# Optimization experiments

Measured on AMD Instinct MI355X. Metric: run time of the kernel, lower is better.

The kernel has to match this reference:

```python
import jax, jax.numpy as jnp
import numpy as np

MIN_V, MAX_V = 1e-7, 10.0
POWER = 2.0
N_NODES = 200000


def _hyper_layer(H, edges, W, b):
    """One HyperTensorGraphConvolution layer (full-neighborhood branch).

    H: [N, d] node signals; edges: [E, S] node indices per hyperedge.
    For each (edge, node_i): power-mean over the other S-1 nodes of the edge,
    divided by (S-1), accumulated onto node_i; then row-normalize and linear.
    """
    N, d = H.shape
    E, S = edges.shape
    H = jnp.clip(H, MIN_V, MAX_V)
    P = H ** POWER                                   # [N, d]
    g = P[edges]                                     # [E, S, d] gather
    edge_sum = g.sum(axis=1, keepdims=True)          # [E, 1, d]
    neigh_mean = (edge_sum - g) / (S - 1)            # exclude self, /(len(nodes)-1)
    contrib = neigh_mean ** (1.0 / POWER)            # [E, S, d]
    add = jax.ops.segment_sum(contrib.reshape(E * S, d),
                              edges.reshape(-1), num_segments=N)
    new_signal = H + add
    # row-normalize (rowsum > 0 because H >= 1e-7)
    rowsum = new_signal.sum(axis=1)
    r_inv = jnp.where(jnp.isfinite(1.0 / rowsum), 1.0 / rowsum, 0.0)
    AH = new_signal * r_inv[:, None]
    return AH @ W + b


def setup_inputs() -> dict:
    key = jax.random.key(0)
    k1, k2, k3, k4, k5, k6 = jax.random.split(key, 6)
    d, h, c = 128, 16, 40
    H = jax.random.uniform(k1, (N_NODES, d), dtype=jnp.float32)
    edges = jax.random.randint(k2, (40000, 16), 0, N_NODES, dtype=jnp.int64)
    std1 = 1.0 / np.sqrt(h)
    std2 = 1.0 / np.sqrt(c)
    W1 = jax.random.uniform(k3, (d, h), jnp.float32, -std1, std1)
    b1 = jax.random.uniform(k4, (h,), jnp.float32, -std1, std1)
    W2 = jax.random.uniform(k5, (h, c), jnp.float32, -std2, std2)
    b2 = jax.random.uniform(k6, (c,), jnp.float32, -std2, std2)
    return {"H": H, "W1": W1, "b1": b1, "W2": W2, "b2": b2, "edges": edges}


def reference(H, W1, b1, W2, b2, edges):
    # layer 1 + relu (dropout is identity in eval mode)
    x = jax.nn.relu(_hyper_layer(H, edges, W1, b1))
    # layer 2
    return _hyper_layer(x, edges, W2, b2)
```

## Files before the change

### kernel.cpp

```cpp
#include <hip/hip_runtime.h>

#define MIN_V 1e-7f
#define MAX_V 10.0f
#define INV15 (1.0f/15.0f)
#define CAP 32

typedef _Float16 half2v __attribute__((ext_vector_type(2)));
typedef _Float16 half4v __attribute__((ext_vector_type(4)));
typedef _Float16 half8v __attribute__((ext_vector_type(8)));

static __device__ __forceinline__ float clipv(float v){
    return fminf(fmaxf(v, MIN_V), MAX_V);
}
static __device__ __forceinline__ float rsqrt_arg(float v){
    return __builtin_amdgcn_sqrtf(fmaxf(v, 0.f));
}

__global__ __launch_bounds__(256) void ch_stream(const float* __restrict__ H,
                                                 _Float16* __restrict__ CH, int total8){
    int stride = gridDim.x*256;
    for (int i = blockIdx.x*256 + threadIdx.x; i < total8; i += stride){
        const float4* p = (const float4*)(H + (size_t)i*8);
        float4 a = p[0], b = p[1];
        half8v o;
        o[0]=(_Float16)clipv(a.x); o[1]=(_Float16)clipv(a.y);
        o[2]=(_Float16)clipv(a.z); o[3]=(_Float16)clipv(a.w);
        o[4]=(_Float16)clipv(b.x); o[5]=(_Float16)clipv(b.y);
        o[6]=(_Float16)clipv(b.z); o[7]=(_Float16)clipv(b.w);
        *(half8v*)(CH + (size_t)i*8) = o;
    }
}

__global__ void build_lists(const int* __restrict__ edges, int* __restrict__ cnt,
                            unsigned short* __restrict__ lists, int total){
    int i = blockIdx.x*256 + threadIdx.x;
    if (i >= total) return;
    int node = edges[i];
    int p = atomicAdd(&cnt[node], 1);
    if (p < CAP) lists[(size_t)node*CAP + p] = (unsigned short)(i >> 4);
}

__global__ __launch_bounds__(256) void es_l1(const _Float16* __restrict__ CH,
                                             const int* __restrict__ edges,
                                             _Float16* __restrict__ ES1s, int E){
    int wave = threadIdx.x >> 6, lane = threadIdx.x & 63;
    int e = blockIdx.x*4 + wave;
    if (e >= E) return;
    int rid = edges[(size_t)e*16 + (lane & 15)];
    float s0 = 0.f, s1 = 0.f;
    #pragma unroll
    for (int s=0;s<16;++s){
        int idx = __shfl(rid, s, 64);
        half2v v = *(const half2v*)(CH + (size_t)idx*128 + lane*2);
        float f0 = (float)v[0], f1 = (float)v[1];
        s0 += f0*f0; s1 += f1*f1;
    }
    half2v o; o[0] = (_Float16)(s0*INV15); o[1] = (_Float16)(s1*INV15);
    *(half2v*)(ES1s + (size_t)e*128 + lane*2) = o;
}

__global__ __launch_bounds__(256) void fused_l1(
    const _Float16* __restrict__ CH, const _Float16* __restrict__ ES1s,
    const int* __restrict__ cnt, const unsigned short* __restrict__ lists,
    const float* __restrict__ W1, const float* __restrict__ b1,
    _Float16* __restrict__ X, int N){
    __shared__ float snw[8*144];
    int tid = threadIdx.x;
    int wave = tid >> 6, lane = tid & 63;

    int q = lane >> 4, h = lane & 15;
    float w[32];
    #pragma unroll
    for (int i=0;i<32;++i) w[i] = W1[(q*32+i)*16 + h];
    float bv = b1[h];

    int hw = tid >> 5;
    int k32 = tid & 31;
    int dq = k32 * 4;

    int nb = blockIdx.x * 8;

    int n = nb + hw;
    if (n < N){
        int myid = (int)lists[(size_t)n*CAP + k32];
        int len = cnt[n]; if (len > CAP) len = CAP;

        half4v hv = *(const half4v*)(CH + (size_t)n*128 + dq);
        float h0=(float)hv[0], h1=(float)hv[1], h2=(float)hv[2], h3=(float)hv[3];
        float p0=h0*h0*INV15, p1=h1*h1*INV15, p2=h2*h2*INV15, p3=h3*h3*INV15;

        float a0=0.f, a1=0.f, a2=0.f, a3=0.f;
        for (int k0=0;k0<len;k0+=4){
            int e0 = __shfl(myid, k0+0, 32);
            int e1 = __shfl(myid, k0+1, 32);
            int e2 = __shfl(myid, k0+2, 32);
            int e3 = __shfl(myid, k0+3, 32);
            half4v v0 = *(const half4v*)(ES1s + (size_t)e0*128 + dq);
            half4v v1 = *(const half4v*)(ES1s + (size_t)e1*128 + dq);
            half4v v2 = *(const half4v*)(ES1s + (size_t)e2*128 + dq);
            half4v v3 = *(const half4v*)(ES1s + (size_t)e3*128 + dq);
            a0 += rsqrt_arg((float)v0[0] - p0);
            a1 += rsqrt_arg((float)v0[1] - p1);
            a2 += rsqrt_arg((float)v0[2] - p2);
            a3 += rsqrt_arg((float)v0[3] - p3);
            bool m1 = (k0+1 < len), m2 = (k0+2 < len), m3 = (k0+3 < len);
            a0 += m1 ? rsqrt_arg((float)v1[0] - p0) : 0.f;
            a1 += m1 ? rsqrt_arg((float)v1[1] - p1) : 0.f;
            a2 += m1 ? rsqrt_arg((float)v1[2] - p2) : 0.f;
            a3 += m1 ? rsqrt_arg((float)v1[3] - p3) : 0.f;
            a0 += m2 ? rsqrt_arg((float)v2[0] - p0) : 0.f;
            a1 += m2 ? rsqrt_arg((float)v2[1] - p1) : 0.f;
            a2 += m2 ? rsqrt_arg((float)v2[2] - p2) : 0.f;
            a3 += m2 ? rsqrt_arg((float)v2[3] - p3) : 0.f;
            a0 += m3 ? rsqrt_arg((float)v3[0] - p0) : 0.f;
            a1 += m3 ? rsqrt_arg((float)v3[1] - p1) : 0.f;
            a2 += m3 ? rsqrt_arg((float)v3[2] - p2) : 0.f;
            a3 += m3 ? rsqrt_arg((float)v3[3] - p3) : 0.f;
        }
        float4 wv;
        wv.x = h0+a0; wv.y = h1+a1; wv.z = h2+a2; wv.w = h3+a3;
        *(float4*)&snw[hw*144 + (k32>>3)*36 + (k32&7)*4] = wv;
    }
    __syncthreads();

    #pragma unroll
    for (int r=0;r<2;++r){
        int nl = wave*2 + r;
        int n2 = nb + nl;
        if (n2 >= N) continue;
        float acc = 0.f, rs = 0.f;
        #pragma unroll
        for (int j=0;j<8;++j){
            float4 v = *(const float4*)&snw[nl*144 + q*36 + j*4];
            acc += v.x*w[j*4+0] + v.y*w[j*4+1] + v.z*w[j*4+2] + v.w*w[j*4+3];
            rs  += v.x + v.y + v.z + v.w;
        }
        acc += __shfl_xor(acc, 16, 64);
        rs  += __shfl_xor(rs , 16, 64);
        acc += __shfl_xor(acc, 32, 64);
        rs  += __shfl_xor(rs , 32, 64);
        if (q == 0){
            float o = acc * __builtin_amdgcn_rcpf(rs) + bv;
            X[(size_t)n2*16 + h] = (_Float16)fmaxf(o, 0.f);
        }
    }
}

__global__ __launch_bounds__(256) void es_l2(const _Float16* __restrict__ X,
                                             const int* __restrict__ edges,
                                             _Float16* __restrict__ ES2s, int E){
    int t = blockIdx.x*256 + threadIdx.x;
    int e = t >> 3, dd2 = (t & 7)*2;
    if (e >= E) return;
    const int* row = edges + (size_t)e*16;
    float s0 = 0.f, s1 = 0.f;
    #pragma unroll
    for (int s=0;s<16;++s){
        half2v v = *(const half2v*)(X + (size_t)row[s]*16 + dd2);
        float f0 = clipv((float)v[0]), f1 = clipv((float)v[1]);
        s0 += f0*f0; s1 += f1*f1;
    }
    half2v o; o[0]=(_Float16)(s0*INV15); o[1]=(_Float16)(s1*INV15);
    *(half2v*)(ES2s + (size_t)e*16 + dd2) = o;
}

__global__ __launch_bounds__(256) void node_l2(
    const _Float16* __restrict__ X, const _Float16* __restrict__ ES2s,
    const int* __restrict__ cnt, const unsigned short* __restrict__ lists,
    const float* __restrict__ W2, const float* __restrict__ b2,
    float* __restrict__ out, int N){
    __shared__ float sW[640];
    __shared__ float sb[40];
    for (int i=threadIdx.x;i<640;i+=256) sW[i] = W2[i];
    if (threadIdx.x < 40) sb[threadIdx.x] = b2[threadIdx.x];
    __syncthreads();
    int n = blockIdx.x*256 + threadIdx.x;
    if (n >= N) return;
    float xc[16], ps[16], ad[16];
    const half8v* xr = (const half8v*)(X + (size_t)n*16);
    half8v x0 = xr[0], x1 = xr[1];
    #pragma unroll
    for (int d=0;d<8;++d){
        float v = clipv((float)x0[d]);
        xc[d]=v; ps[d]=v*v*INV15; ad[d]=0.f;
    }
    #pragma unroll
    for (int d=0;d<8;++d){
        float v = clipv((float)x1[d]);
        xc[8+d]=v; ps[8+d]=v*v*INV15; ad[8+d]=0.f;
    }
    int len = cnt[n]; if (len > CAP) len = CAP;
    const unsigned short* lrow = lists + (size_t)n*CAP;
    for (int k0=0;k0<len;k0+=2){
        int e0 = lrow[k0];
        int e1 = (k0+1 < len) ? lrow[k0+1] : e0;
        bool m1 = (k0+1 < len);
        const half8v* r0 = (const half8v*)(ES2s + (size_t)e0*16);
        const half8v* r1 = (const half8v*)(ES2s + (size_t)e1*16);
        half8v ea0 = r0[0], eb0 = r0[1];
        half8v ea1 = r1[0], eb1 = r1[1];
        #pragma unroll
        for (int d=0;d<8;++d){
            ad[d]   += rsqrt_arg((float)ea0[d] - ps[d]);
            ad[8+d] += rsqrt_arg((float)eb0[d] - ps[8+d]);
        }
        #pragma unroll
        for (int d=0;d<8;++d){
            ad[d]   += m1 ? rsqrt_arg((float)ea1[d] - ps[d])   : 0.f;
            ad[8+d] += m1 ? rsqrt_arg((float)eb1[d] - ps[8+d]) : 0.f;
        }
    }
    float rs = 0.f;
    float nw[16];
    #pragma unroll
    for (int d=0;d<16;++d){ nw[d] = xc[d] + ad[d]; rs += nw[d]; }
    float rinv = __builtin_amdgcn_rcpf(rs);
    float acc[40];
    #pragma unroll
    for (int c=0;c<40;++c) acc[c] = 0.f;
    #pragma unroll
    for (int d=0;d<16;++d){
        float v = nw[d];
        #pragma unroll
        for (int c=0;c<40;++c) acc[c] += v * sW[d*40+c];
    }
    float4 ob[10];
    #pragma unroll
    for (int c=0;c<40;++c) ((float*)ob)[c] = rinv*acc[c] + sb[c];
    float4* op = (float4*)(out + (size_t)n*40);
    #pragma unroll
    for (int j=0;j<10;++j) op[j] = ob[j];
}

extern "C" void kernel_launch(void* const* d_in, const int* in_sizes, int n_in,
                              void* d_out, int out_size, void* d_ws, size_t ws_size,
                              hipStream_t stream){
    (void)n_in; (void)out_size; (void)ws_size;
    const float* H  = (const float*)d_in[0];
    const float* W1 = (const float*)d_in[1];
    const float* b1 = (const float*)d_in[2];
    const float* W2 = (const float*)d_in[3];
    const float* b2 = (const float*)d_in[4];
    const int* edges = (const int*)d_in[5];
    float* out = (float*)d_out;

    const int N = in_sizes[0] / 128;
    const int E = in_sizes[5] / 16;
    const int total = E * 16;
    const int total8 = N * 128 / 8;

    char* ws = (char*)d_ws;
    size_t off = 0;
    _Float16* CH   = (_Float16*)(ws + off);
    _Float16* X    = (_Float16*)(ws + off);
    _Float16* ES2s = (_Float16*)(ws + off + (size_t)N*16*sizeof(_Float16));
    off += (size_t)N*128*sizeof(_Float16);
    _Float16* ES1s = (_Float16*)(ws + off); off += (size_t)E*128*sizeof(_Float16);
    int* cnt = (int*)(ws + off); off += (size_t)N*sizeof(int);
    unsigned short* lists = (unsigned short*)(ws + off);
    off += (size_t)N*CAP*sizeof(unsigned short);

    hipMemsetAsync(cnt, 0, (size_t)N*sizeof(int), stream);
    ch_stream<<<2048, 256, 0, stream>>>(H, CH, total8);
    build_lists<<<(total+255)/256, 256, 0, stream>>>(edges, cnt, lists, total);
    es_l1<<<(E+3)/4, 256, 0, stream>>>(CH, edges, ES1s, E);
    fused_l1<<<(N+7)/8, 256, 0, stream>>>(CH, ES1s, cnt, lists, W1, b1, X, N);
    es_l2<<<(E*8+255)/256, 256, 0, stream>>>(X, edges, ES2s, E);
    node_l2<<<(N+255)/256, 256, 0, stream>>>(X, ES2s, cnt, lists, W2, b2, out, N);
}
```

Before: 197.0 us.

## Move power-mean and linear layers to packed fp16 math with zero-edge padding

Replaces the fp32 sqrt/subtract work in both node-aggregation kernels with packed half-precision vector max/sqrt, and the small matmuls with fdot2 instructions on fp16 weights. Padding is now handled by a sentinel zero row appended to the edge-sum buffers, so the per-element masks go away. The edge-sum kernels process four features per thread instead of two, and the workspace layout changes so X no longer aliases CH. This trims ALU and register pressure at the cost of lower intermediate precision, which may affect tolerance.

```diff
diff --git a/kernel.cpp b/kernel.cpp
--- a/kernel.cpp
+++ b/kernel.cpp
@@ -11,9 +11,6 @@
 
 static __device__ __forceinline__ float clipv(float v){
     return fminf(fmaxf(v, MIN_V), MAX_V);
-}
-static __device__ __forceinline__ float rsqrt_arg(float v){
-    return __builtin_amdgcn_sqrtf(fmaxf(v, 0.f));
 }
 
 __global__ __launch_bounds__(256) void ch_stream(const float* __restrict__ H,
@@ -43,83 +40,84 @@
 __global__ __launch_bounds__(256) void es_l1(const _Float16* __restrict__ CH,
                                              const int* __restrict__ edges,
                                              _Float16* __restrict__ ES1s, int E){
-    int wave = threadIdx.x >> 6, lane = threadIdx.x & 63;
-    int e = blockIdx.x*4 + wave;
+    int tid = threadIdx.x;
+    int hw = tid >> 5, l32 = tid & 31;
+    int e = blockIdx.x*8 + hw;
     if (e >= E) return;
-    int rid = edges[(size_t)e*16 + (lane & 15)];
-    float s0 = 0.f, s1 = 0.f;
+    int nid = edges[(size_t)e*16 + (l32 & 15)];
+    int dq = l32 * 4;
+    float s0=0.f, s1=0.f, s2=0.f, s3=0.f;
     #pragma unroll
     for (int s=0;s<16;++s){
-        int idx = __shfl(rid, s, 64);
-        half2v v = *(const half2v*)(CH + (size_t)idx*128 + lane*2);
-        float f0 = (float)v[0], f1 = (float)v[1];
-        s0 += f0*f0; s1 += f1*f1;
-    }
-    half2v o; o[0] = (_Float16)(s0*INV15); o[1] = (_Float16)(s1*INV15);
-    *(half2v*)(ES1s + (size_t)e*128 + lane*2) = o;
+        int idx = __shfl(nid, s, 32);
+        half4v v = *(const half4v*)(CH + (size_t)idx*128 + dq);
+        float f0=(float)v[0], f1=(float)v[1], f2=(float)v[2], f3=(float)v[3];
+        s0 += f0*f0; s1 += f1*f1; s2 += f2*f2; s3 += f3*f3;
+    }
+    half4v o;
+    o[0]=(_Float16)(s0*INV15); o[1]=(_Float16)(s1*INV15);
+    o[2]=(_Float16)(s2*INV15); o[3]=(_Float16)(s3*INV15);
+    *(half4v*)(ES1s + (size_t)e*128 + dq) = o;
 }
 
 __global__ __launch_bounds__(256) void fused_l1(
     const _Float16* __restrict__ CH, const _Float16* __restrict__ ES1s,
     const int* __restrict__ cnt, const unsigned short* __restrict__ lists,
     const float* __restrict__ W1, const float* __restrict__ b1,
-    _Float16* __restrict__ X, int N){
-    __shared__ float snw[8*144];
+    _Float16* __restrict__ X, int N, int EZERO){
+    __shared__ _Float16 snw[8*128];
     int tid = threadIdx.x;
     int wave = tid >> 6, lane = tid & 63;
 
     int q = lane >> 4, h = lane & 15;
-    float w[32];
-    #pragma unroll
-    for (int i=0;i<32;++i) w[i] = W1[(q*32+i)*16 + h];
+    half2v w2[16];
+    #pragma unroll
+    for (int i=0;i<16;++i){
+        w2[i][0] = (_Float16)W1[(q*32+2*i  )*16 + h];
+        w2[i][1] = (_Float16)W1[(q*32+2*i+1)*16 + h];
+    }
+    const half2v ones = {(_Float16)1.f, (_Float16)1.f};
     float bv = b1[h];
 
     int hw = tid >> 5;
     int k32 = tid & 31;
     int dq = k32 * 4;
-
     int nb = blockIdx.x * 8;
 
     int n = nb + hw;
     if (n < N){
+        int len = cnt[n]; if (len > CAP) len = CAP;
         int myid = (int)lists[(size_t)n*CAP + k32];
-        int len = cnt[n]; if (len > CAP) len = CAP;
+        myid = (k32 < len) ? myid : EZERO;
 
         half4v hv = *(const half4v*)(CH + (size_t)n*128 + dq);
-        float h0=(float)hv[0], h1=(float)hv[1], h2=(float)hv[2], h3=(float)hv[3];
-        float p0=h0*h0*INV15, p1=h1*h1*INV15, p2=h2*h2*INV15, p3=h3*h3*INV15;
+        const _Float16 i15 = (_Float16)INV15;
+        half4v i15v = {i15, i15, i15, i15};
+        half4v p16 = (hv * hv) * i15v;
+        const half4v z4 = {(_Float16)0.f,(_Float16)0.f,(_Float16)0.f,(_Float16)0.f};
 
         float a0=0.f, a1=0.f, a2=0.f, a3=0.f;
-        for (int k0=0;k0<len;k0+=4){
-            int e0 = __shfl(myid, k0+0, 32);
+        int iters = (len + 1) & ~1;
+        for (int k0=0;k0<iters;k0+=2){
+            int e0 = __shfl(myid, k0,   32);
             int e1 = __shfl(myid, k0+1, 32);
-            int e2 = __shfl(myid, k0+2, 32);
-            int e3 = __shfl(myid, k0+3, 32);
             half4v v0 = *(const half4v*)(ES1s + (size_t)e0*128 + dq);
             half4v v1 = *(const half4v*)(ES1s + (size_t)e1*128 + dq);
-            half4v v2 = *(const half4v*)(ES1s + (size_t)e2*128 + dq);
-            half4v v3 = *(const half4v*)(ES1s + (size_t)e3*128 + dq);
-            a0 += rsqrt_arg((float)v0[0] - p0);
-            a1 += rsqrt_arg((float)v0[1] - p1);
-            a2 += rsqrt_arg((float)v0[2] - p2);
-            a3 += rsqrt_arg((float)v0[3] - p3);
-            bool m1 = (k0+1 < len), m2 = (k0+2 < len), m3 = (k0+3 < len);
-            a0 += m1 ? rsqrt_arg((float)v1[0] - p0) : 0.f;
-            a1 += m1 ? rsqrt_arg((float)v1[1] - p1) : 0.f;
-            a2 += m1 ? rsqrt_arg((float)v1[2] - p2) : 0.f;
-            a3 += m1 ? rsqrt_arg((float)v1[3] - p3) : 0.f;
-            a0 += m2 ? rsqrt_arg((float)v2[0] - p0) : 0.f;
-            a1 += m2 ? rsqrt_arg((float)v2[1] - p1) : 0.f;
-            a2 += m2 ? rsqrt_arg((float)v2[2] - p2) : 0.f;
-            a3 += m2 ? rsqrt_arg((float)v2[3] - p3) : 0.f;
-            a0 += m3 ? rsqrt_arg((float)v3[0] - p0) : 0.f;
-            a1 += m3 ? rsqrt_arg((float)v3[1] - p1) : 0.f;
-            a2 += m3 ? rsqrt_arg((float)v3[2] - p2) : 0.f;
-            a3 += m3 ? rsqrt_arg((float)v3[3] - p3) : 0.f;
-        }
-        float4 wv;
-        wv.x = h0+a0; wv.y = h1+a1; wv.z = h2+a2; wv.w = h3+a3;
-        *(float4*)&snw[hw*144 + (k32>>3)*36 + (k32&7)*4] = wv;
+            half4v m0 = __builtin_elementwise_max(v0 - p16, z4);
+            half4v m1 = __builtin_elementwise_max(v1 - p16, z4);
+            half4v s0 = __builtin_elementwise_sqrt(m0);
+            half4v s1 = __builtin_elementwise_sqrt(m1);
+            a0 += (float)s0[0] + (float)s1[0];
+            a1 += (float)s0[1] + (float)s1[1];
+            a2 += (float)s0[2] + (float)s1[2];
+            a3 += (float)s0[3] + (float)s1[3];
+        }
+        half4v o;
+        o[0] = (_Float16)((float)hv[0] + a0);
+        o[1] = (_Float16)((float)hv[1] + a1);
+        o[2] = (_Float16)((float)hv[2] + a2);
+        o[3] = (_Float16)((float)hv[3] + a3);
+        *(half4v*)&snw[hw*128 + dq] = o;
     }
     __syncthreads();
 
@@ -131,9 +129,12 @@
         float acc = 0.f, rs = 0.f;
         #pragma unroll
         for (int j=0;j<8;++j){
-            float4 v = *(const float4*)&snw[nl*144 + q*36 + j*4];
-            acc += v.x*w[j*4+0] + v.y*w[j*4+1] + v.z*w[j*4+2] + v.w*w[j*4+3];
-            rs  += v.x + v.y + v.z + v.w;
+            half4v v = *(const half4v*)&snw[nl*128 + q*32 + j*4];
+            half2v lo = {v[0], v[1]}, hi = {v[2], v[3]};
+            acc = __builtin_amdgcn_fdot2(lo, w2[j*2  ], acc, false);
+            acc = __builtin_amdgcn_fdot2(hi, w2[j*2+1], acc, false);
+            rs  = __builtin_amdgcn_fdot2(lo, ones, rs, false);
+            rs  = __builtin_amdgcn_fdot2(hi, ones, rs, false);
         }
         acc += __shfl_xor(acc, 16, 64);
         rs  += __shfl_xor(rs , 16, 64);
@@ -150,64 +151,76 @@
                                              const int* __restrict__ edges,
                                              _Float16* __restrict__ ES2s, int E){
     int t = blockIdx.x*256 + threadIdx.x;
-    int e = t >> 3, dd2 = (t & 7)*2;
+    int e = t >> 2, dq = (t & 3)*4;
     if (e >= E) return;
     const int* row = edges + (size_t)e*16;
-    float s0 = 0.f, s1 = 0.f;
+    const _Float16 c7 = (_Float16)1e-7f;
+    const half4v c7v = {c7, c7, c7, c7};
+    float s0=0.f, s1=0.f, s2=0.f, s3=0.f;
     #pragma unroll
     for (int s=0;s<16;++s){
-        half2v v = *(const half2v*)(X + (size_t)row[s]*16 + dd2);
-        float f0 = clipv((float)v[0]), f1 = clipv((float)v[1]);
-        s0 += f0*f0; s1 += f1*f1;
-    }
-    half2v o; o[0]=(_Float16)(s0*INV15); o[1]=(_Float16)(s1*INV15);
-    *(half2v*)(ES2s + (size_t)e*16 + dd2) = o;
+        half4v v = *(const half4v*)(X + (size_t)row[s]*16 + dq);
+        v = __builtin_elementwise_max(v, c7v);
+        float f0=(float)v[0], f1=(float)v[1], f2=(float)v[2], f3=(float)v[3];
+        s0 += f0*f0; s1 += f1*f1; s2 += f2*f2; s3 += f3*f3;
+    }
+    half4v o;
+    o[0]=(_Float16)(s0*INV15); o[1]=(_Float16)(s1*INV15);
+    o[2]=(_Float16)(s2*INV15); o[3]=(_Float16)(s3*INV15);
+    *(half4v*)(ES2s + (size_t)e*16 + dq) = o;
 }
 
 __global__ __launch_bounds__(256) void node_l2(
     const _Float16* __restrict__ X, const _Float16* __restrict__ ES2s,
     const int* __restrict__ cnt, const unsigned short* __restrict__ lists,
     const float* __restrict__ W2, const float* __restrict__ b2,
-    float* __restrict__ out, int N){
-    __shared__ float sW[640];
+    float* __restrict__ out, int N, int EZERO){
+    __shared__ half2v sW2h[8*40];
     __shared__ float sb[40];
-    for (int i=threadIdx.x;i<640;i+=256) sW[i] = W2[i];
+    for (int i=threadIdx.x;i<320;i+=256){
+        int d2 = i/40, c = i - d2*40;
+        half2v wp;
+        wp[0] = (_Float16)W2[(2*d2  )*40 + c];
+        wp[1] = (_Float16)W2[(2*d2+1)*40 + c];
+        sW2h[i] = wp;
+    }
     if (threadIdx.x < 40) sb[threadIdx.x] = b2[threadIdx.x];
     __syncthreads();
     int n = blockIdx.x*256 + threadIdx.x;
     if (n >= N) return;
-    float xc[16], ps[16], ad[16];
+
+    const _Float16 c7 = (_Float16)1e-7f;
+    const half8v c7v = {c7,c7,c7,c7,c7,c7,c7,c7};
+    const half8v z8 = {(_Float16)0.f,(_Float16)0.f,(_Float16)0.f,(_Float16)0.f,
+                       (_Float16)0.f,(_Float16)0.f,(_Float16)0.f,(_Float16)0.f};
+    const _Float16 i15 = (_Float16)INV15;
+    const half8v i15v = {i15,i15,i15,i15,i15,i15,i15,i15};
+
     const half8v* xr = (const half8v*)(X + (size_t)n*16);
-    half8v x0 = xr[0], x1 = xr[1];
-    #pragma unroll
-    for (int d=0;d<8;++d){
-        float v = clipv((float)x0[d]);
-        xc[d]=v; ps[d]=v*v*INV15; ad[d]=0.f;
-    }
-    #pragma unroll
-    for (int d=0;d<8;++d){
-        float v = clipv((float)x1[d]);
-        xc[8+d]=v; ps[8+d]=v*v*INV15; ad[8+d]=0.f;
-    }
+    half8v x0 = __builtin_elementwise_max(xr[0], c7v);
+    half8v x1 = __builtin_elementwise_max(xr[1], c7v);
+    half8v ps0 = (x0*x0)*i15v;
+    half8v ps1 = (x1*x1)*i15v;
+
+    float xc[16], ad[16];
+    #pragma unroll
+    for (int d=0;d<8;++d){ xc[d]=(float)x0[d]; xc[8+d]=(float)x1[d]; ad[d]=0.f; ad[8+d]=0.f; }
+
     int len = cnt[n]; if (len > CAP) len = CAP;
     const unsigned short* lrow = lists + (size_t)n*CAP;
     for (int k0=0;k0<len;k0+=2){
         int e0 = lrow[k0];
-        int e1 = (k0+1 < len) ? lrow[k0+1] : e0;
-        bool m1 = (k0+1 < len);
+        int e1 = (k0+1 < len) ? (int)lrow[k0+1] : EZERO;
         const half8v* r0 = (const half8v*)(ES2s + (size_t)e0*16);
         const half8v* r1 = (const half8v*)(ES2s + (size_t)e1*16);
-        half8v ea0 = r0[0], eb0 = r0[1];
-        half8v ea1 = r1[0], eb1 = r1[1];
+        half8v sa0 = __builtin_elementwise_sqrt(__builtin_elementwise_max(r0[0]-ps0, z8));
+        half8v sb0 = __builtin_elementwise_sqrt(__builtin_elementwise_max(r0[1]-ps1, z8));
+        half8v sa1 = __builtin_elementwise_sqrt(__builtin_elementwise_max(r1[0]-ps0, z8));
+        half8v sb1 = __builtin_elementwise_sqrt(__builtin_elementwise_max(r1[1]-ps1, z8));
         #pragma unroll
         for (int d=0;d<8;++d){
-            ad[d]   += rsqrt_arg((float)ea0[d] - ps[d]);
-            ad[8+d] += rsqrt_arg((float)eb0[d] - ps[8+d]);
-        }
-        #pragma unroll
-        for (int d=0;d<8;++d){
-            ad[d]   += m1 ? rsqrt_arg((float)ea1[d] - ps[d])   : 0.f;
-            ad[8+d] += m1 ? rsqrt_arg((float)eb1[d] - ps[8+d]) : 0.f;
+            ad[d]   += (float)sa0[d] + (float)sa1[d];
+            ad[8+d] += (float)sb0[d] + (float)sb1[d];
         }
     }
     float rs = 0.f;
@@ -215,18 +228,20 @@
     #pragma unroll
     for (int d=0;d<16;++d){ nw[d] = xc[d] + ad[d]; rs += nw[d]; }
     float rinv = __builtin_amdgcn_rcpf(rs);
-    float acc[40];
-    #pragma unroll
-    for (int c=0;c<40;++c) acc[c] = 0.f;
-    #pragma unroll
-    for (int d=0;d<16;++d){
-        float v = nw[d];
+
+    half2v nwh[8];
+    #pragma unroll
+    for (int i=0;i<8;++i){ nwh[i][0] = (_Float16)nw[2*i]; nwh[i][1] = (_Float16)nw[2*i+1]; }
+
+    float4 ob[10];
+    #pragma unroll
+    for (int c=0;c<40;++c){
+        float acc = 0.f;
         #pragma unroll
-        for (int c=0;c<40;++c) acc[c] += v * sW[d*40+c];
-    }
-    float4 ob[10];
-    #pragma unroll
-    for (int c=0;c<40;++c) ((float*)ob)[c] = rinv*acc[c] + sb[c];
+        for (int d2=0;d2<8;++d2)
+            acc = __builtin_amdgcn_fdot2(nwh[d2], sW2h[d2*40+c], acc, false);
+        ((float*)ob)[c] = rinv*acc + sb[c];
+    }
     float4* op = (float4*)(out + (size_t)n*40);
     #pragma unroll
     for (int j=0;j<10;++j) op[j] = ob[j];
@@ -252,19 +267,21 @@
     char* ws = (char*)d_ws;
     size_t off = 0;
     _Float16* CH   = (_Float16*)(ws + off);
-    _Float16* X    = (_Float16*)(ws + off);
-    _Float16* ES2s = (_Float16*)(ws + off + (size_t)N*16*sizeof(_Float16));
+    _Float16* ES2s = (_Float16*)(ws + off);
     off += (size_t)N*128*sizeof(_Float16);
-    _Float16* ES1s = (_Float16*)(ws + off); off += (size_t)E*128*sizeof(_Float16);
+    _Float16* ES1s = (_Float16*)(ws + off); off += (size_t)(E+1)*128*sizeof(_Float16);
+    _Float16* X    = (_Float16*)(ws + off); off += (size_t)N*16*sizeof(_Float16);
     int* cnt = (int*)(ws + off); off += (size_t)N*sizeof(int);
     unsigned short* lists = (unsigned short*)(ws + off);
     off += (size_t)N*CAP*sizeof(unsigned short);
 
     hipMemsetAsync(cnt, 0, (size_t)N*sizeof(int), stream);
+    hipMemsetAsync(ES1s + (size_t)E*128, 0, 128*sizeof(_Float16), stream);
     ch_stream<<<2048, 256, 0, stream>>>(H, CH, total8);
     build_lists<<<(total+255)/256, 256, 0, stream>>>(edges, cnt, lists, total);
-    es_l1<<<(E+3)/4, 256, 0, stream>>>(CH, edges, ES1s, E);
-    fused_l1<<<(N+7)/8, 256, 0, stream>>>(CH, ES1s, cnt, lists, W1, b1, X, N);
-    es_l2<<<(E*8+255)/256, 256, 0, stream>>>(X, edges, ES2s, E);
-    node_l2<<<(N+255)/256, 256, 0, stream>>>(X, ES2s, cnt, lists, W2, b2, out, N);
-}
+    es_l1<<<(E+7)/8, 256, 0, stream>>>(CH, edges, ES1s, E);
+    fused_l1<<<(N+7)/8, 256, 0, stream>>>(CH, ES1s, cnt, lists, W1, b1, X, N, E);
+    hipMemsetAsync(ES2s + (size_t)E*16, 0, 16*sizeof(_Float16), stream);
+    es_l2<<<(E*4+255)/256, 256, 0, stream>>>(X, edges, ES2s, E);
+    node_l2<<<(N+255)/256, 256, 0, stream>>>(X, ES2s, cnt, lists, W2, b2, out, N, E);
+}
```

Result: no change. 199.9 us (+1.5%).

## Compute layer-1 neighbor aggregation in packed fp16 with zero-edge padding sentinel

Applied to the files above, without the earlier changes.

The layer-1 node kernel now does subtract, clamp, sqrt and accumulate in packed half4 arithmetic, and its projection uses fp16 dot2 instructions. Per-iteration masks are replaced by a padded all-zero sentinel edge row that is read for slots past the list length. Layer-2 edge sums are stored as fp32 instead of fp16, and the workspace is reorganised so X and ES2s no longer alias. The aim is to cut VALU work and conversions in the hot gather loop, at the cost of lower accumulation precision in layer 1 and twice the bytes for layer-2 edge reads.

```diff
diff --git a/kernel.cpp b/kernel.cpp
--- a/kernel.cpp
+++ b/kernel.cpp
@@ -63,35 +63,42 @@
     const _Float16* __restrict__ CH, const _Float16* __restrict__ ES1s,
     const int* __restrict__ cnt, const unsigned short* __restrict__ lists,
     const float* __restrict__ W1, const float* __restrict__ b1,
-    _Float16* __restrict__ X, int N){
-    __shared__ float snw[8*144];
+    _Float16* __restrict__ X, int N, int EZERO){
+    __shared__ _Float16 snw[8*128];
     int tid = threadIdx.x;
     int wave = tid >> 6, lane = tid & 63;
 
     int q = lane >> 4, h = lane & 15;
-    float w[32];
-    #pragma unroll
-    for (int i=0;i<32;++i) w[i] = W1[(q*32+i)*16 + h];
+    half2v w2[16];
+    #pragma unroll
+    for (int i=0;i<16;++i){
+        w2[i][0] = (_Float16)W1[(q*32+2*i  )*16 + h];
+        w2[i][1] = (_Float16)W1[(q*32+2*i+1)*16 + h];
+    }
+    const half2v ones = {(_Float16)1.f, (_Float16)1.f};
     float bv = b1[h];
 
     int hw = tid >> 5;
     int k32 = tid & 31;
     int dq = k32 * 4;
-
     int nb = blockIdx.x * 8;
+
+    const _Float16 i15 = (_Float16)INV15;
+    const half4v i15v = {i15, i15, i15, i15};
+    const half4v z4 = {(_Float16)0.f,(_Float16)0.f,(_Float16)0.f,(_Float16)0.f};
 
     int n = nb + hw;
     if (n < N){
+        int len = cnt[n]; if (len > CAP) len = CAP;
         int myid = (int)lists[(size_t)n*CAP + k32];
-        int len = cnt[n]; if (len > CAP) len = CAP;
+        myid = (k32 < len) ? myid : EZERO;
 
         half4v hv = *(const half4v*)(CH + (size_t)n*128 + dq);
-        float h0=(float)hv[0], h1=(float)hv[1], h2=(float)hv[2], h3=(float)hv[3];
-        float p0=h0*h0*INV15, p1=h1*h1*INV15, p2=h2*h2*INV15, p3=h3*h3*INV15;
-
-        float a0=0.f, a1=0.f, a2=0.f, a3=0.f;
+        half4v p16 = (hv * hv) * i15v;
+
+        half4v acc = z4;
         for (int k0=0;k0<len;k0+=4){
-            int e0 = __shfl(myid, k0+0, 32);
+            int e0 = __shfl(myid, k0,   32);
             int e1 = __shfl(myid, k0+1, 32);
             int e2 = __shfl(myid, k0+2, 32);
             int e3 = __shfl(myid, k0+3, 32);
@@ -99,27 +106,12 @@
             half4v v1 = *(const half4v*)(ES1s + (size_t)e1*128 + dq);
             half4v v2 = *(const half4v*)(ES1s + (size_t)e2*128 + dq);
             half4v v3 = *(const half4v*)(ES1s + (size_t)e3*128 + dq);
-            a0 += rsqrt_arg((float)v0[0] - p0);
-            a1 += rsqrt_arg((float)v0[1] - p1);
-            a2 += rsqrt_arg((float)v0[2] - p2);
-            a3 += rsqrt_arg((float)v0[3] - p3);
-            bool m1 = (k0+1 < len), m2 = (k0+2 < len), m3 = (k0+3 < len);
-            a0 += m1 ? rsqrt_arg((float)v1[0] - p0) : 0.f;
-            a1 += m1 ? rsqrt_arg((float)v1[1] - p1) : 0.f;
-            a2 += m1 ? rsqrt_arg((float)v1[2] - p2) : 0.f;
-            a3 += m1 ? rsqrt_arg((float)v1[3] - p3) : 0.f;
-            a0 += m2 ? rsqrt_arg((float)v2[0] - p0) : 0.f;
-            a1 += m2 ? rsqrt_arg((float)v2[1] - p1) : 0.f;
-            a2 += m2 ? rsqrt_arg((float)v2[2] - p2) : 0.f;
-            a3 += m2 ? rsqrt_arg((float)v2[3] - p3) : 0.f;
-            a0 += m3 ? rsqrt_arg((float)v3[0] - p0) : 0.f;
-            a1 += m3 ? rsqrt_arg((float)v3[1] - p1) : 0.f;
-            a2 += m3 ? rsqrt_arg((float)v3[2] - p2) : 0.f;
-            a3 += m3 ? rsqrt_arg((float)v3[3] - p3) : 0.f;
-        }
-        float4 wv;
-        wv.x = h0+a0; wv.y = h1+a1; wv.z = h2+a2; wv.w = h3+a3;
-        *(float4*)&snw[hw*144 + (k32>>3)*36 + (k32&7)*4] = wv;
+            acc = acc + __builtin_elementwise_sqrt(__builtin_elementwise_max(v0 - p16, z4));
+            acc = acc + __builtin_elementwise_sqrt(__builtin_elementwise_max(v1 - p16, z4));
+            acc = acc + __builtin_elementwise_sqrt(__builtin_elementwise_max(v2 - p16, z4));
+            acc = acc + __builtin_elementwise_sqrt(__builtin_elementwise_max(v3 - p16, z4));
+        }
+        *(half4v*)&snw[hw*128 + dq] = hv + acc;
     }
     __syncthreads();
 
@@ -131,9 +123,12 @@
         float acc = 0.f, rs = 0.f;
         #pragma unroll
         for (int j=0;j<8;++j){
-            float4 v = *(const float4*)&snw[nl*144 + q*36 + j*4];
-            acc += v.x*w[j*4+0] + v.y*w[j*4+1] + v.z*w[j*4+2] + v.w*w[j*4+3];
-            rs  += v.x + v.y + v.z + v.w;
+            half4v v = *(const half4v*)&snw[nl*128 + q*32 + j*4];
+            half2v lo = {v[0], v[1]}, hi = {v[2], v[3]};
+            acc = __builtin_amdgcn_fdot2(lo, w2[j*2  ], acc, false);
+            acc = __builtin_amdgcn_fdot2(hi, w2[j*2+1], acc, false);
+            rs  = __builtin_amdgcn_fdot2(lo, ones, rs, false);
+            rs  = __builtin_amdgcn_fdot2(hi, ones, rs, false);
         }
         acc += __shfl_xor(acc, 16, 64);
         rs  += __shfl_xor(rs , 16, 64);
@@ -148,7 +143,7 @@
 
 __global__ __launch_bounds__(256) void es_l2(const _Float16* __restrict__ X,
                                              const int* __restrict__ edges,
-                                             _Float16* __restrict__ ES2s, int E){
+                                             float* __restrict__ ES2s, int E){
     int t = blockIdx.x*256 + threadIdx.x;
     int e = t >> 3, dd2 = (t & 7)*2;
     if (e >= E) return;
@@ -160,12 +155,12 @@
         float f0 = clipv((float)v[0]), f1 = clipv((float)v[1]);
         s0 += f0*f0; s1 += f1*f1;
     }
-    half2v o; o[0]=(_Float16)(s0*INV15); o[1]=(_Float16)(s1*INV15);
-    *(half2v*)(ES2s + (size_t)e*16 + dd2) = o;
+    ES2s[(size_t)e*16 + dd2]     = s0*INV15;
+    ES2s[(size_t)e*16 + dd2 + 1] = s1*INV15;
 }
 
 __global__ __launch_bounds__(256) void node_l2(
-    const _Float16* __restrict__ X, const _Float16* __restrict__ ES2s,
+    const _Float16* __restrict__ X, const float* __restrict__ ES2s,
     const int* __restrict__ cnt, const unsigned short* __restrict__ lists,
     const float* __restrict__ W2, const float* __restrict__ b2,
     float* __restrict__ out, int N){
@@ -195,19 +190,19 @@
         int e0 = lrow[k0];
         int e1 = (k0+1 < len) ? lrow[k0+1] : e0;
         bool m1 = (k0+1 < len);
-        const half8v* r0 = (const half8v*)(ES2s + (size_t)e0*16);
-        const half8v* r1 = (const half8v*)(ES2s + (size_t)e1*16);
-        half8v ea0 = r0[0], eb0 = r0[1];
-        half8v ea1 = r1[0], eb1 = r1[1];
+        const float4* r0 = (const float4*)(ES2s + (size_t)e0*16);
+        const float4* r1 = (const float4*)(ES2s + (size_t)e1*16);
         #pragma unroll
-        for (int d=0;d<8;++d){
-            ad[d]   += rsqrt_arg((float)ea0[d] - ps[d]);
-            ad[8+d] += rsqrt_arg((float)eb0[d] - ps[8+d]);
-        }
-        #pragma unroll
-        for (int d=0;d<8;++d){
-            ad[d]   += m1 ? rsqrt_arg((float)ea1[d] - ps[d])   : 0.f;
-            ad[8+d] += m1 ? rsqrt_arg((float)eb1[d] - ps[8+d]) : 0.f;
+        for (int j=0;j<4;++j){
+            float4 ea = r0[j], eb = r1[j];
+            ad[j*4+0] += rsqrt_arg(ea.x - ps[j*4+0]);
+            ad[j*4+1] += rsqrt_arg(ea.y - ps[j*4+1]);
+            ad[j*4+2] += rsqrt_arg(ea.z - ps[j*4+2]);
+            ad[j*4+3] += rsqrt_arg(ea.w - ps[j*4+3]);
+            ad[j*4+0] += m1 ? rsqrt_arg(eb.x - ps[j*4+0]) : 0.f;
+            ad[j*4+1] += m1 ? rsqrt_arg(eb.y - ps[j*4+1]) : 0.f;
+            ad[j*4+2] += m1 ? rsqrt_arg(eb.z - ps[j*4+2]) : 0.f;
+            ad[j*4+3] += m1 ? rsqrt_arg(eb.w - ps[j*4+3]) : 0.f;
         }
     }
     float rs = 0.f;
@@ -251,20 +246,21 @@
 
     char* ws = (char*)d_ws;
     size_t off = 0;
-    _Float16* CH   = (_Float16*)(ws + off);
-    _Float16* X    = (_Float16*)(ws + off);
-    _Float16* ES2s = (_Float16*)(ws + off + (size_t)N*16*sizeof(_Float16));
+    _Float16* CH  = (_Float16*)(ws + off);
+    float* ES2s   = (float*)(ws + off);
     off += (size_t)N*128*sizeof(_Float16);
-    _Float16* ES1s = (_Float16*)(ws + off); off += (size_t)E*128*sizeof(_Float16);
+    _Float16* ES1s = (_Float16*)(ws + off); off += (size_t)(E+1)*128*sizeof(_Float16);
+    _Float16* X    = (_Float16*)(ws + off); off += (size_t)N*16*sizeof(_Float16);
     int* cnt = (int*)(ws + off); off += (size_t)N*sizeof(int);
     unsigned short* lists = (unsigned short*)(ws + off);
     off += (size_t)N*CAP*sizeof(unsigned short);
 
     hipMemsetAsync(cnt, 0, (size_t)N*sizeof(int), stream);
+    hipMemsetAsync(ES1s + (size_t)E*128, 0, 128*sizeof(_Float16), stream);
     ch_stream<<<2048, 256, 0, stream>>>(H, CH, total8);
     build_lists<<<(total+255)/256, 256, 0, stream>>>(edges, cnt, lists, total);
     es_l1<<<(E+3)/4, 256, 0, stream>>>(CH, edges, ES1s, E);
-    fused_l1<<<(N+7)/8, 256, 0, stream>>>(CH, ES1s, cnt, lists, W1, b1, X, N);
+    fused_l1<<<(N+7)/8, 256, 0, stream>>>(CH, ES1s, cnt, lists, W1, b1, X, N, E);
     es_l2<<<(E*8+255)/256, 256, 0, stream>>>(X, edges, ES2s, E);
     node_l2<<<(N+255)/256, 256, 0, stream>>>(X, ES2s, cnt, lists, W2, b2, out, N);
 }
```

New measurement: 210.1 us. 1.07x slower.
